# Kernel optimization log

Measured on AMD Instinct MI355X. Metric: run time of the kernel, lower is better.

## Reference

```python
import jax, jax.numpy as jnp
import numpy as np

MARGIN = 0.3


def setup_inputs() -> dict:
    key = jax.random.key(0)
    k1, k2 = jax.random.split(key)
    B, D, N_IDS = 8192, 256, 512
    emb = jax.random.normal(k1, (B, D), dtype=jnp.float32)
    emb = emb / jnp.linalg.norm(emb, axis=1, keepdims=True)  # L2-normalized as docstring states
    labels = jax.random.randint(k2, (B,), 0, N_IDS, dtype=jnp.int64)
    return {"embeddings": emb, "labels": labels}


def reference(embeddings, labels):
    B = embeddings.shape[0]
    # pairwise Euclidean distance via cosine similarity (embeddings are L2-normalized)
    sim = jnp.matmul(embeddings, embeddings.T)              # (B, B)
    dist = jnp.sqrt(jnp.clip(2.0 - 2.0 * sim, 0.0) + 1e-12)
    same = labels[:, None] == labels[None, :]               # (B, B)
    eye = jnp.eye(B, dtype=bool)
    pos_mask = same & ~eye
    neg_mask = ~same
    neg_inf = jnp.asarray(-jnp.inf, dist.dtype)
    pos_inf = jnp.asarray(jnp.inf, dist.dtype)
    dist_ap = jnp.max(jnp.where(pos_mask, dist, neg_inf), axis=1)  # hardest positive per anchor
    dist_an = jnp.min(jnp.where(neg_mask, dist, pos_inf), axis=1)  # hardest negative per anchor
    valid = jnp.any(pos_mask, axis=1) & jnp.any(neg_mask, axis=1)
    # MarginRankingLoss(dist_an, dist_ap, y=1) = mean(relu(dist_ap - dist_an + margin)) over valid anchors
    per = jnp.maximum(dist_ap - dist_an + MARGIN, 0.0)
    per = jnp.where(valid, per, 0.0)
    n_valid = jnp.sum(valid.astype(dist.dtype))
    loss = jnp.where(n_valid > 0, jnp.sum(per) / jnp.maximum(n_valid, 1.0), 0.0)
    return loss
```

## Files before the change

kernel.cpp:

```cpp
#include <hip/hip_runtime.h>
#include <hip/hip_bf16.h>


#define BDIM 8192
#define DDIM 256

typedef short bf16x8 __attribute__((ext_vector_type(8)));
typedef float f32x4  __attribute__((ext_vector_type(4)));
typedef unsigned short u16;

static __device__ __forceinline__ bf16x8 ld_frag(const u16* p) {
    return *reinterpret_cast<const bf16x8*>(p);
}

static __device__ __forceinline__ u16 f2bf(float f) {
    union { float f; unsigned int u; } x; x.f = f;
    unsigned int u = x.u;
    unsigned int r = u + 0x7fffu + ((u >> 16) & 1u);
    return (u16)(r >> 16);
}

static __device__ __forceinline__ void gload_lds16(const u16* g, u16* l) {
    __builtin_amdgcn_global_load_lds(
        (const __attribute__((address_space(1))) unsigned int*)g,
        (__attribute__((address_space(3))) unsigned int*)l, 16, 0, 0);
}

__global__ __launch_bounds__(256) void cvt_init_kernel(const float* __restrict__ in,
                                                       u16* __restrict__ out,
                                                       int* __restrict__ minpos,
                                                       int* __restrict__ maxneg) {
    int i = blockIdx.x * 256 + threadIdx.x;
    const float4 v = reinterpret_cast<const float4*>(in)[i];
    ushort4 o;
    o.x = f2bf(v.x); o.y = f2bf(v.y); o.z = f2bf(v.z); o.w = f2bf(v.w);
    reinterpret_cast<ushort4*>(out)[i] = o;
    if (i < BDIM) {
        minpos[i] = 0x7f800000;
        maxneg[i] = 0;
    }
}

__global__ __launch_bounds__(256, 2) void triplet_main(const u16* __restrict__ Ebf,
                                                       const int* __restrict__ labels,
                                                       int* __restrict__ minpos,
                                                       int* __restrict__ maxneg) {
    __shared__ __align__(16) u16 smem[2][32 * DDIM];

    const int tid  = threadIdx.x;
    const int w    = tid >> 6;
    const int l    = tid & 63;
    const int quad = l >> 4;
    const int r16  = l & 15;

    const int mblk  = blockIdx.x * 256 + w * 64;
    const int nbase = blockIdx.y * 512;

    bf16x8 a[4][8];
#pragma unroll
    for (int ms = 0; ms < 4; ++ms) {
        const u16* ap = Ebf + (size_t)(mblk + ms * 16 + r16) * DDIM + quad * 8;
#pragma unroll
        for (int k = 0; k < 8; ++k) a[ms][k] = ld_frag(ap + k * 32);
    }

    int lab_row[4][4];
#pragma unroll
    for (int ms = 0; ms < 4; ++ms)
#pragma unroll
        for (int r = 0; r < 4; ++r)
            lab_row[ms][r] = labels[mblk + ms * 16 + quad * 4 + r];

    float minp[4][4], maxn[4][4];
#pragma unroll
    for (int ms = 0; ms < 4; ++ms)
#pragma unroll
        for (int r = 0; r < 4; ++r) { minp[ms][r] = __builtin_inff(); maxn[ms][r] = -__builtin_inff(); }

    const int qs = quad ^ (r16 & 3);
    const int s4 = (r16 >> 2) & 1;

#pragma unroll
    for (int it = 0; it < 4; ++it) {
        const int q = it * 256 + tid;
        const int r = q >> 5;
        const int c = (q & 31) ^ (r & 7);
        gload_lds16(Ebf + ((size_t)(nbase + r) << 8) + c * 8,
                    &smem[0][0] + it * 2048 + w * 512);
    }

    for (int nn = 0; nn < 16; ++nn) {
        const int cur = nn & 1;
        const int n0  = nbase + nn * 32;

        __syncthreads();

        if (nn + 1 < 16) {
            const int n1 = n0 + 32;
#pragma unroll
            for (int it = 0; it < 4; ++it) {
                const int q = it * 256 + tid;
                const int r = q >> 5;
                const int c = (q & 31) ^ (r & 7);
                gload_lds16(Ebf + ((size_t)(n1 + r) << 8) + c * 8,
                            &smem[cur ^ 1][0] + it * 2048 + w * 512);
            }
        }

        f32x4 acc[4][2];
#pragma unroll
        for (int ms = 0; ms < 4; ++ms)
#pragma unroll
            for (int nt = 0; nt < 2; ++nt)
                acc[ms][nt] = (f32x4){0.f, 0.f, 0.f, 0.f};

        const u16* bb = &smem[cur][0];
        const u16* bnt[2];
#pragma unroll
        for (int nt = 0; nt < 2; ++nt)
            bnt[nt] = bb + (nt * 16 + r16) * DDIM + qs * 8;

#pragma unroll
        for (int k = 0; k < 8; ++k) {
            const int koff = ((k ^ s4) << 5);
            bf16x8 b[2];
#pragma unroll
            for (int nt = 0; nt < 2; ++nt) b[nt] = ld_frag(bnt[nt] + koff);
#pragma unroll
            for (int ms = 0; ms < 4; ++ms)
#pragma unroll
                for (int nt = 0; nt < 2; ++nt)
                    acc[ms][nt] = __builtin_amdgcn_mfma_f32_16x16x32_bf16(
                        a[ms][k], b[nt], acc[ms][nt], 0, 0, 0);
        }

        int lab_c[2];
#pragma unroll
        for (int nt = 0; nt < 2; ++nt) lab_c[nt] = labels[n0 + nt * 16 + r16];

        const bool diagTile = (n0 < mblk + 64) && (mblk < n0 + 32);
        if (__builtin_expect(diagTile, 0)) {
#pragma unroll
            for (int nt = 0; nt < 2; ++nt) {
                const int colg = n0 + nt * 16 + r16;
#pragma unroll
                for (int ms = 0; ms < 4; ++ms)
#pragma unroll
                    for (int r = 0; r < 4; ++r) {
                        const int rowg = mblk + ms * 16 + quad * 4 + r;
                        const float s = acc[ms][nt][r];
                        const bool same = (lab_c[nt] == lab_row[ms][r]);
                        const bool pos  = same && (colg != rowg);
                        minp[ms][r] = fminf(minp[ms][r], pos  ?  s : __builtin_inff());
                        maxn[ms][r] = fmaxf(maxn[ms][r], same ? -__builtin_inff() : s);
                    }
            }
        } else {
#pragma unroll
            for (int nt = 0; nt < 2; ++nt)
#pragma unroll
                for (int ms = 0; ms < 4; ++ms)
#pragma unroll
                    for (int r = 0; r < 4; ++r) {
                        const float s = acc[ms][nt][r];
                        const bool same = (lab_c[nt] == lab_row[ms][r]);
                        minp[ms][r] = fminf(minp[ms][r], same ?  s : __builtin_inff());
                        maxn[ms][r] = fmaxf(maxn[ms][r], same ? -__builtin_inff() : s);
                    }
        }
    }

#pragma unroll
    for (int mask = 1; mask <= 8; mask <<= 1) {
#pragma unroll
        for (int ms = 0; ms < 4; ++ms)
#pragma unroll
            for (int r = 0; r < 4; ++r) {
                minp[ms][r] = fminf(minp[ms][r], __shfl_xor(minp[ms][r], mask, 64));
                maxn[ms][r] = fmaxf(maxn[ms][r], __shfl_xor(maxn[ms][r], mask, 64));
            }
    }
    if (r16 == 0) {
#pragma unroll
        for (int ms = 0; ms < 4; ++ms)
#pragma unroll
            for (int r = 0; r < 4; ++r) {
                const int rowg = mblk + ms * 16 + quad * 4 + r;
                atomicMin(minpos + rowg, __float_as_int(minp[ms][r] + 2.0f));
                atomicMax(maxneg + rowg, __float_as_int(maxn[ms][r] + 2.0f));
            }
    }
}

__global__ __launch_bounds__(1024) void finalize_kernel(const int* __restrict__ minpos,
                                                        const int* __restrict__ maxneg,
                                                        float* __restrict__ out) {
    __shared__ float ssum[16], scnt[16];
    float sum = 0.f, cnt = 0.f;
#pragma unroll
    for (int it = 0; it < 8; ++it) {
        const int i = it * 1024 + threadIdx.x;
        const float mp = __int_as_float(minpos[i]);
        const float mn = __int_as_float(maxneg[i]);
        if (mp < 1e30f && mn > 0.5f) {
            const float dap = sqrtf(fmaxf(6.0f - 2.0f * mp, 0.0f) + 1e-12f);
            const float dan = sqrtf(fmaxf(6.0f - 2.0f * mn, 0.0f) + 1e-12f);
            sum += fmaxf(dap - dan + 0.3f, 0.0f);
            cnt += 1.0f;
        }
    }
#pragma unroll
    for (int off = 32; off > 0; off >>= 1) {
        sum += __shfl_down(sum, off, 64);
        cnt += __shfl_down(cnt, off, 64);
    }
    const int wid = threadIdx.x >> 6;
    if ((threadIdx.x & 63) == 0) { ssum[wid] = sum; scnt[wid] = cnt; }
    __syncthreads();
    if (threadIdx.x == 0) {
        float S = 0.f, C = 0.f;
#pragma unroll
        for (int i = 0; i < 16; ++i) { S += ssum[i]; C += scnt[i]; }
        out[0] = (C > 0.f) ? (S / C) : 0.f;
    }
}

extern "C" void kernel_launch(void* const* d_in, const int* in_sizes, int n_in,
                              void* d_out, int out_size, void* d_ws, size_t ws_size,
                              hipStream_t stream) {
    const float* emb    = (const float*)d_in[0];
    const int*   labels = (const int*)d_in[1];
    float*       out    = (float*)d_out;

    u16* Ebf    = (u16*)d_ws;
    int* minpos = (int*)((char*)d_ws + (size_t)BDIM * DDIM * 2);
    int* maxneg = minpos + BDIM;

    cvt_init_kernel<<<dim3((BDIM * DDIM / 4) / 256), dim3(256), 0, stream>>>(emb, Ebf, minpos, maxneg);
    triplet_main<<<dim3(BDIM / 256, BDIM / 512), dim3(256), 0, stream>>>(Ebf, labels, minpos, maxneg);
    finalize_kernel<<<dim3(1), dim3(1024), 0, stream>>>(minpos, maxneg, out);
}
```

Baseline: 105.2 us.

## Exploit Gram matrix symmetry: compute upper-triangle tiles and reduce rows and columns

Uses the symmetry of E·Eᵀ to compute only the 528 upper-triangular 256x256 tiles instead of all 1024. Each tile updates the row-wise min-positive and max-negative as before, and also reduces column-wise extrema into LDS via shared atomics, then flushes them with global atomics. This roughly halves the MFMA and load work. In exchange it adds per-tile cross-lane shuffles, LDS atomics, extra global atomics and a serial tile-index decode loop at block start. Diagonal tiles handle self-exclusion for both directions through the existing diagTile path.

```diff
diff --git a/kernel.cpp b/kernel.cpp
--- a/kernel.cpp
+++ b/kernel.cpp
@@ -46,6 +46,8 @@
                                                        int* __restrict__ minpos,
                                                        int* __restrict__ maxneg) {
     __shared__ __align__(16) u16 smem[2][32 * DDIM];
+    __shared__ int colmin[256], colmax[256];
+    __shared__ int labc[256];
 
     const int tid  = threadIdx.x;
     const int w    = tid >> 6;
@@ -53,8 +55,16 @@
     const int quad = l >> 4;
     const int r16  = l & 15;
 
-    const int mblk  = blockIdx.x * 256 + w * 64;
-    const int nbase = blockIdx.y * 512;
+    int idx = blockIdx.x, pi = 0, base = 0;
+    while (idx >= base + (32 - pi)) { base += (32 - pi); ++pi; }
+    const int pj = pi + (idx - base);
+
+    const int mblk  = pi * 256 + w * 64;
+    const int jbase = pj * 256;
+
+    colmin[tid] = 0x7f800000;
+    colmax[tid] = 0;
+    labc[tid]   = labels[jbase + tid];
 
     bf16x8 a[4][8];
 #pragma unroll
@@ -85,17 +95,19 @@
         const int q = it * 256 + tid;
         const int r = q >> 5;
         const int c = (q & 31) ^ (r & 7);
-        gload_lds16(Ebf + ((size_t)(nbase + r) << 8) + c * 8,
+        gload_lds16(Ebf + ((size_t)(jbase + r) << 8) + c * 8,
                     &smem[0][0] + it * 2048 + w * 512);
     }
 
-    for (int nn = 0; nn < 16; ++nn) {
+    const f32x4 zero4 = (f32x4){0.f, 0.f, 0.f, 0.f};
+
+    for (int nn = 0; nn < 8; ++nn) {
         const int cur = nn & 1;
-        const int n0  = nbase + nn * 32;
+        const int n0  = jbase + nn * 32;
 
         __syncthreads();
 
-        if (nn + 1 < 16) {
+        if (nn + 1 < 8) {
             const int n1 = n0 + 32;
 #pragma unroll
             for (int it = 0; it < 4; ++it) {
@@ -108,20 +120,26 @@
         }
 
         f32x4 acc[4][2];
-#pragma unroll
-        for (int ms = 0; ms < 4; ++ms)
-#pragma unroll
-            for (int nt = 0; nt < 2; ++nt)
-                acc[ms][nt] = (f32x4){0.f, 0.f, 0.f, 0.f};
-
         const u16* bb = &smem[cur][0];
         const u16* bnt[2];
 #pragma unroll
         for (int nt = 0; nt < 2; ++nt)
             bnt[nt] = bb + (nt * 16 + r16) * DDIM + qs * 8;
 
-#pragma unroll
-        for (int k = 0; k < 8; ++k) {
+        {
+            const int koff = ((0 ^ s4) << 5);
+            bf16x8 b[2];
+#pragma unroll
+            for (int nt = 0; nt < 2; ++nt) b[nt] = ld_frag(bnt[nt] + koff);
+#pragma unroll
+            for (int ms = 0; ms < 4; ++ms)
+#pragma unroll
+                for (int nt = 0; nt < 2; ++nt)
+                    acc[ms][nt] = __builtin_amdgcn_mfma_f32_16x16x32_bf16(
+                        a[ms][0], b[nt], zero4, 0, 0, 0);
+        }
+#pragma unroll
+        for (int k = 1; k < 8; ++k) {
             const int koff = ((k ^ s4) << 5);
             bf16x8 b[2];
 #pragma unroll
@@ -134,14 +152,14 @@
                         a[ms][k], b[nt], acc[ms][nt], 0, 0, 0);
         }
 
-        int lab_c[2];
-#pragma unroll
-        for (int nt = 0; nt < 2; ++nt) lab_c[nt] = labels[n0 + nt * 16 + r16];
-
         const bool diagTile = (n0 < mblk + 64) && (mblk < n0 + 32);
-        if (__builtin_expect(diagTile, 0)) {
-#pragma unroll
-            for (int nt = 0; nt < 2; ++nt) {
+#pragma unroll
+        for (int nt = 0; nt < 2; ++nt) {
+            const int ci    = nn * 32 + nt * 16 + r16;
+            const int lab_c = labc[ci - nn * 32 + nn * 32];
+            float cmin =  __builtin_inff();
+            float cmax = -__builtin_inff();
+            if (__builtin_expect(diagTile, 0)) {
                 const int colg = n0 + nt * 16 + r16;
 #pragma unroll
                 for (int ms = 0; ms < 4; ++ms)
@@ -149,24 +167,38 @@
                     for (int r = 0; r < 4; ++r) {
                         const int rowg = mblk + ms * 16 + quad * 4 + r;
                         const float s = acc[ms][nt][r];
-                        const bool same = (lab_c[nt] == lab_row[ms][r]);
+                        const bool same = (lab_c == lab_row[ms][r]);
                         const bool pos  = same && (colg != rowg);
-                        minp[ms][r] = fminf(minp[ms][r], pos  ?  s : __builtin_inff());
-                        maxn[ms][r] = fmaxf(maxn[ms][r], same ? -__builtin_inff() : s);
+                        const float v = pos  ?  s : __builtin_inff();
+                        const float x = same ? -__builtin_inff() : s;
+                        minp[ms][r] = fminf(minp[ms][r], v);
+                        maxn[ms][r] = fmaxf(maxn[ms][r], x);
+                        cmin = fminf(cmin, v);
+                        cmax = fmaxf(cmax, x);
                     }
-            }
-        } else {
-#pragma unroll
-            for (int nt = 0; nt < 2; ++nt)
+            } else {
 #pragma unroll
                 for (int ms = 0; ms < 4; ++ms)
 #pragma unroll
                     for (int r = 0; r < 4; ++r) {
                         const float s = acc[ms][nt][r];
-                        const bool same = (lab_c[nt] == lab_row[ms][r]);
-                        minp[ms][r] = fminf(minp[ms][r], same ?  s : __builtin_inff());
-                        maxn[ms][r] = fmaxf(maxn[ms][r], same ? -__builtin_inff() : s);
+                        const bool same = (lab_c == lab_row[ms][r]);
+                        const float v = same ?  s : __builtin_inff();
+                        const float x = same ? -__builtin_inff() : s;
+                        minp[ms][r] = fminf(minp[ms][r], v);
+                        maxn[ms][r] = fmaxf(maxn[ms][r], x);
+                        cmin = fminf(cmin, v);
+                        cmax = fmaxf(cmax, x);
                     }
+            }
+            cmin = fminf(cmin, __shfl_xor(cmin, 16, 64));
+            cmin = fminf(cmin, __shfl_xor(cmin, 32, 64));
+            cmax = fmaxf(cmax, __shfl_xor(cmax, 16, 64));
+            cmax = fmaxf(cmax, __shfl_xor(cmax, 32, 64));
+            if (quad == 0) {
+                atomicMin(&colmin[ci], __float_as_int(cmin + 2.0f));
+                atomicMax(&colmax[ci], __float_as_int(cmax + 2.0f));
+            }
         }
     }
 
@@ -190,6 +222,10 @@
                 atomicMax(maxneg + rowg, __float_as_int(maxn[ms][r] + 2.0f));
             }
     }
+
+    __syncthreads();
+    atomicMin(minpos + jbase + tid, colmin[tid]);
+    atomicMax(maxneg + jbase + tid, colmax[tid]);
 }
 
 __global__ __launch_bounds__(1024) void finalize_kernel(const int* __restrict__ minpos,
@@ -237,6 +273,6 @@
     int* maxneg = minpos + BDIM;
 
     cvt_init_kernel<<<dim3((BDIM * DDIM / 4) / 256), dim3(256), 0, stream>>>(emb, Ebf, minpos, maxneg);
-    triplet_main<<<dim3(BDIM / 256, BDIM / 512), dim3(256), 0, stream>>>(Ebf, labels, minpos, maxneg);
+    triplet_main<<<dim3(528), dim3(256), 0, stream>>>(Ebf, labels, minpos, maxneg);
     finalize_kernel<<<dim3(1), dim3(1024), 0, stream>>>(minpos, maxneg, out);
 }
```

New measurement: 118.3 us. +12.4%, slower.

## Widen LDS swizzle, issue tile prefetch earlier, vectorize bf16 conversion

Applied to the files above, without the earlier changes.

The B-tile LDS swizzle now XORs the chunk index with the full row index instead of its low three bits. The fragment reads use per-lane k-offsets (r16>>2 and 4+(r16>>2)) so the two n-subtiles hit different banks. The first tile prefetch is issued before the A-fragment register loads, so global-to-LDS traffic overlaps them. The first MFMA takes a zero accumulator instead of an explicit zeroing loop, and the conversion kernel now processes 8 floats per thread with packed 32-bit stores. The swizzle change carries a correctness risk if the read-side permutation does not exactly match the write-side one.

```diff
diff --git a/kernel.cpp b/kernel.cpp
--- a/kernel.cpp
+++ b/kernel.cpp
@@ -8,16 +8,16 @@
 typedef short bf16x8 __attribute__((ext_vector_type(8)));
 typedef float f32x4  __attribute__((ext_vector_type(4)));
 typedef unsigned short u16;
+typedef unsigned int u32;
 
 static __device__ __forceinline__ bf16x8 ld_frag(const u16* p) {
     return *reinterpret_cast<const bf16x8*>(p);
 }
 
-static __device__ __forceinline__ u16 f2bf(float f) {
-    union { float f; unsigned int u; } x; x.f = f;
-    unsigned int u = x.u;
-    unsigned int r = u + 0x7fffu + ((u >> 16) & 1u);
-    return (u16)(r >> 16);
+static __device__ __forceinline__ u32 f2bf(float f) {
+    union { float f; u32 u; } x; x.f = f;
+    u32 u = x.u;
+    return (u + 0x7fffu + ((u >> 16) & 1u)) >> 16;
 }
 
 static __device__ __forceinline__ void gload_lds16(const u16* g, u16* l) {
@@ -30,11 +30,16 @@
                                                        u16* __restrict__ out,
                                                        int* __restrict__ minpos,
                                                        int* __restrict__ maxneg) {
-    int i = blockIdx.x * 256 + threadIdx.x;
-    const float4 v = reinterpret_cast<const float4*>(in)[i];
-    ushort4 o;
-    o.x = f2bf(v.x); o.y = f2bf(v.y); o.z = f2bf(v.z); o.w = f2bf(v.w);
-    reinterpret_cast<ushort4*>(out)[i] = o;
+    const int i = blockIdx.x * 256 + threadIdx.x;
+    const float4* in4 = reinterpret_cast<const float4*>(in);
+    const float4 v0 = in4[2 * i];
+    const float4 v1 = in4[2 * i + 1];
+    uint4 o;
+    o.x = f2bf(v0.x) | (f2bf(v0.y) << 16);
+    o.y = f2bf(v0.z) | (f2bf(v0.w) << 16);
+    o.z = f2bf(v1.x) | (f2bf(v1.y) << 16);
+    o.w = f2bf(v1.z) | (f2bf(v1.w) << 16);
+    reinterpret_cast<uint4*>(out)[i] = o;
     if (i < BDIM) {
         minpos[i] = 0x7f800000;
         maxneg[i] = 0;
@@ -56,38 +61,41 @@
     const int mblk  = blockIdx.x * 256 + w * 64;
     const int nbase = blockIdx.y * 512;
 
-    bf16x8 a[4][8];
-#pragma unroll
-    for (int ms = 0; ms < 4; ++ms) {
-        const u16* ap = Ebf + (size_t)(mblk + ms * 16 + r16) * DDIM + quad * 8;
-#pragma unroll
-        for (int k = 0; k < 8; ++k) a[ms][k] = ld_frag(ap + k * 32);
-    }
-
-    int lab_row[4][4];
-#pragma unroll
-    for (int ms = 0; ms < 4; ++ms)
-#pragma unroll
-        for (int r = 0; r < 4; ++r)
-            lab_row[ms][r] = labels[mblk + ms * 16 + quad * 4 + r];
-
-    float minp[4][4], maxn[4][4];
-#pragma unroll
-    for (int ms = 0; ms < 4; ++ms)
-#pragma unroll
-        for (int r = 0; r < 4; ++r) { minp[ms][r] = __builtin_inff(); maxn[ms][r] = -__builtin_inff(); }
-
-    const int qs = quad ^ (r16 & 3);
-    const int s4 = (r16 >> 2) & 1;
-
 #pragma unroll
     for (int it = 0; it < 4; ++it) {
         const int q = it * 256 + tid;
         const int r = q >> 5;
-        const int c = (q & 31) ^ (r & 7);
+        const int c = (q & 31) ^ r;
         gload_lds16(Ebf + ((size_t)(nbase + r) << 8) + c * 8,
                     &smem[0][0] + it * 2048 + w * 512);
     }
+
+    bf16x8 a[4][8];
+#pragma unroll
+    for (int ms = 0; ms < 4; ++ms) {
+        const u16* ap = Ebf + (size_t)(mblk + ms * 16 + r16) * DDIM + quad * 8;
+#pragma unroll
+        for (int k = 0; k < 8; ++k) a[ms][k] = ld_frag(ap + k * 32);
+    }
+
+    int lab_row[4][4];
+#pragma unroll
+    for (int ms = 0; ms < 4; ++ms)
+#pragma unroll
+        for (int r = 0; r < 4; ++r)
+            lab_row[ms][r] = labels[mblk + ms * 16 + quad * 4 + r];
+
+    float minp[4][4], maxn[4][4];
+#pragma unroll
+    for (int ms = 0; ms < 4; ++ms)
+#pragma unroll
+        for (int r = 0; r < 4; ++r) { minp[ms][r] = __builtin_inff(); maxn[ms][r] = -__builtin_inff(); }
+
+    const int qs  = quad ^ (r16 & 3);
+    const int kx0 = (r16 >> 2);
+    const int kx1 = 4 + kx0;
+
+    const f32x4 zero4 = (f32x4){0.f, 0.f, 0.f, 0.f};
 
     for (int nn = 0; nn < 16; ++nn) {
         const int cur = nn & 1;
@@ -101,42 +109,42 @@
             for (int it = 0; it < 4; ++it) {
                 const int q = it * 256 + tid;
                 const int r = q >> 5;
-                const int c = (q & 31) ^ (r & 7);
+                const int c = (q & 31) ^ r;
                 gload_lds16(Ebf + ((size_t)(n1 + r) << 8) + c * 8,
                             &smem[cur ^ 1][0] + it * 2048 + w * 512);
             }
         }
 
+        int lab_c[2];
+#pragma unroll
+        for (int nt = 0; nt < 2; ++nt) lab_c[nt] = labels[n0 + nt * 16 + r16];
+
         f32x4 acc[4][2];
-#pragma unroll
-        for (int ms = 0; ms < 4; ++ms)
-#pragma unroll
-            for (int nt = 0; nt < 2; ++nt)
-                acc[ms][nt] = (f32x4){0.f, 0.f, 0.f, 0.f};
-
         const u16* bb = &smem[cur][0];
         const u16* bnt[2];
 #pragma unroll
         for (int nt = 0; nt < 2; ++nt)
             bnt[nt] = bb + (nt * 16 + r16) * DDIM + qs * 8;
 
-#pragma unroll
-        for (int k = 0; k < 8; ++k) {
-            const int koff = ((k ^ s4) << 5);
-            bf16x8 b[2];
-#pragma unroll
-            for (int nt = 0; nt < 2; ++nt) b[nt] = ld_frag(bnt[nt] + koff);
-#pragma unroll
-            for (int ms = 0; ms < 4; ++ms)
-#pragma unroll
-                for (int nt = 0; nt < 2; ++nt)
-                    acc[ms][nt] = __builtin_amdgcn_mfma_f32_16x16x32_bf16(
-                        a[ms][k], b[nt], acc[ms][nt], 0, 0, 0);
-        }
-
-        int lab_c[2];
-#pragma unroll
-        for (int nt = 0; nt < 2; ++nt) lab_c[nt] = labels[n0 + nt * 16 + r16];
+        {
+            bf16x8 b0 = ld_frag(bnt[0] + ((0 ^ kx0) << 5));
+            bf16x8 b1 = ld_frag(bnt[1] + ((0 ^ kx1) << 5));
+#pragma unroll
+            for (int ms = 0; ms < 4; ++ms) {
+                acc[ms][0] = __builtin_amdgcn_mfma_f32_16x16x32_bf16(a[ms][0], b0, zero4, 0, 0, 0);
+                acc[ms][1] = __builtin_amdgcn_mfma_f32_16x16x32_bf16(a[ms][0], b1, zero4, 0, 0, 0);
+            }
+        }
+#pragma unroll
+        for (int k = 1; k < 8; ++k) {
+            bf16x8 b0 = ld_frag(bnt[0] + ((k ^ kx0) << 5));
+            bf16x8 b1 = ld_frag(bnt[1] + ((k ^ kx1) << 5));
+#pragma unroll
+            for (int ms = 0; ms < 4; ++ms) {
+                acc[ms][0] = __builtin_amdgcn_mfma_f32_16x16x32_bf16(a[ms][k], b0, acc[ms][0], 0, 0, 0);
+                acc[ms][1] = __builtin_amdgcn_mfma_f32_16x16x32_bf16(a[ms][k], b1, acc[ms][1], 0, 0, 0);
+            }
+        }
 
         const bool diagTile = (n0 < mblk + 64) && (mblk < n0 + 32);
         if (__builtin_expect(diagTile, 0)) {
@@ -236,7 +244,7 @@
     int* minpos = (int*)((char*)d_ws + (size_t)BDIM * DDIM * 2);
     int* maxneg = minpos + BDIM;
 
-    cvt_init_kernel<<<dim3((BDIM * DDIM / 4) / 256), dim3(256), 0, stream>>>(emb, Ebf, minpos, maxneg);
+    cvt_init_kernel<<<dim3((BDIM * DDIM / 8) / 256), dim3(256), 0, stream>>>(emb, Ebf, minpos, maxneg);
     triplet_main<<<dim3(BDIM / 256, BDIM / 512), dim3(256), 0, stream>>>(Ebf, labels, minpos, maxneg);
     finalize_kernel<<<dim3(1), dim3(1024), 0, stream>>>(minpos, maxneg, out);
 }
```

After: 105.9 us. Within noise of the previous version (+0.6%).
